# Optimization experiments

Hardware: AMD Instinct MI355X
Metric: run time of the kernel (lower is better)

The kernel has to match this reference:

```python
import jax, jax.numpy as jnp
import numpy as np

GH = 256       # GRU hidden size
VOCAB = 1000
MAX_EP = 150
NPREV = NCURR = NNEXT = 64


def _gru_scan(emb, h0, wih, whh, bih, bhh):
    # torch nn.GRU single-layer math, scanned over the token axis
    H = h0.shape[0]
    def step(h, x_t):
        gi = wih @ x_t + bih            # [3H]
        gh = whh @ h + bhh              # [3H]
        r = jax.nn.sigmoid(gi[:H] + gh[:H])
        z = jax.nn.sigmoid(gi[H:2 * H] + gh[H:2 * H])
        n = jnp.tanh(gi[2 * H:] + r * gh[2 * H:])
        hn = (1.0 - z) * n + z * h
        return hn, hn
    _, hs = jax.lax.scan(step, h0, emb)
    return hs                            # [L, H]


def _conv(x, w, b, s):
    y = jax.lax.conv_general_dilated(x, w, (s, s), 'VALID',
                                     dimension_numbers=('NCHW', 'OIHW', 'NCHW'))
    return y + b[None, :, None, None]


def setup_inputs():
    key = jax.random.key(0)
    ks = jax.random.split(key, 48)
    f32 = jnp.float32
    def W(i, shape, s=0.05):
        return (jax.random.normal(ks[i], shape) * s).astype(f32)
    inp = dict(
        x=jax.random.normal(ks[0], (1, 3, 124, 124), f32),
        hx=jax.random.normal(ks[1], (1, 256), f32),
        cx=jax.random.normal(ks[2], (1, 256), f32),
        conv1_w=W(3, (128, 3, 8, 8)), conv1_b=jnp.zeros((128,), f32),
        conv2_w=W(4, (64, 128, 4, 4)), conv2_b=jnp.zeros((64,), f32),
        conv3_w=W(5, (64, 64, 4, 4)), conv3_b=jnp.zeros((64,), f32),
        emb_w=W(6, (VOCAB, 32), 1.0),
        gru_f_wih=W(7, (3 * GH, 32)), gru_f_whh=W(8, (3 * GH, GH)),
        gru_f_bih=jnp.zeros((3 * GH,), f32), gru_f_bhh=jnp.zeros((3 * GH,), f32),
        gru_b_wih=W(9, (3 * GH, 32)), gru_b_whh=W(10, (3 * GH, GH)),
        gru_b_bih=jnp.zeros((3 * GH,), f32), gru_b_bhh=jnp.zeros((3 * GH,), f32),
        time_emb_w=W(11, (MAX_EP + 1, 32), 1.0),
        temp_emb_w=W(12, (2, 32), 1.0),
        img_emb_w=W(13, (256, 64 * 6 * 6)), img_emb_b=jnp.zeros((256,), f32),
        attn_key_w=W(14, (256, 256 * 3)), attn_key_b=jnp.zeros((256,), f32),
        bilinear_A=W(15, (1, 256, 544)), bilinear_b=jnp.zeros((1,), f32),
        reduce_w=W(16, (128, 544)), reduce_b=jnp.zeros((128,), f32),
        gate_w=W(17, (64, 640)), gate_b=jnp.zeros((64,), f32),
        lin_w=W(18, (256, 64 * 6 * 6)), lin_b=jnp.zeros((256,), f32),
        lstm_wih=W(19, (1024, 256)), lstm_whh=W(20, (1024, 256)),
        lstm_bih=jnp.zeros((1024,), f32), lstm_bhh=jnp.zeros((1024,), f32),
        critic_w=W(21, (1, 288)), critic_b=jnp.zeros((1,), f32),
        actor_w=W(22, (4, 288)), actor_b=jnp.zeros((4,), f32),
        prev_inst=jax.random.randint(ks[23], (1, NPREV), 0, VOCAB),
        curr_inst=jax.random.randint(ks[24], (1, NCURR), 0, VOCAB),
        next_inst=jax.random.randint(ks[25], (1, NNEXT), 0, VOCAB),
        tx=jax.random.randint(ks[26], (1,), 0, MAX_EP + 1),
    )
    return inp


def reference(x, hx, cx, conv1_w, conv1_b, conv2_w, conv2_b, conv3_w, conv3_b,
              emb_w, gru_f_wih, gru_f_whh, gru_f_bih, gru_f_bhh,
              gru_b_wih, gru_b_whh, gru_b_bih, gru_b_bhh,
              time_emb_w, temp_emb_w, img_emb_w, img_emb_b,
              attn_key_w, attn_key_b, bilinear_A, bilinear_b,
              reduce_w, reduce_b, gate_w, gate_b, lin_w, lin_b,
              lstm_wih, lstm_whh, lstm_bih, lstm_bhh,
              critic_w, critic_b, actor_w, actor_b,
              prev_inst, curr_inst, next_inst, tx):
    np_, nc, nn_ = prev_inst.shape[1], curr_inst.shape[1], next_inst.shape[1]
    all_inst = jnp.concatenate([prev_inst, curr_inst, next_inst], axis=1)[0]  # [L]
    L = all_inst.shape[0]

    # CNN encoder
    h = jax.nn.relu(_conv(x, conv1_w, conv1_b, 4))
    h = jax.nn.relu(_conv(h, conv2_w, conv2_b, 2))
    x_img = jax.nn.relu(_conv(h, conv3_w, conv3_b, 2))       # [1,64,6,6]

    # token-looped GRUs -> single lax.scan each (note: original runs gru_b
    # over the SAME forward order then reverses the hidden list; replicated)
    emb = emb_w[all_inst]                                    # [L,32]
    h0 = jnp.zeros((GH,), emb.dtype)
    hs_f = _gru_scan(emb, h0, gru_f_wih, gru_f_whh, gru_f_bih, gru_f_bhh)
    hs_b = _gru_scan(emb, h0, gru_b_wih, gru_b_whh, gru_b_bih, gru_b_bhh)[::-1]
    curr_instr_rep = jnp.concatenate([hs_f[np_ + nc - 1], hs_b[np_]])[None]  # [1,512]
    ir_f = jnp.concatenate([hs_f[:np_], hs_f[L - nn_:]], axis=0)             # [M,256]
    ir_b = jnp.concatenate([hs_b[:np_], hs_b[L - nn_:]], axis=0)
    temp_tok = jnp.concatenate([jnp.zeros((np_,), jnp.int32), jnp.ones((nn_,), jnp.int32)])
    instr_rep = jnp.concatenate([ir_f, ir_b, temp_emb_w[temp_tok]], axis=1)  # [M,544]

    # bilinear attention over prev/next token states
    image_emb = x_img.reshape(1, -1) @ img_emb_w.T + img_emb_b               # [1,256]
    attn_key = jnp.concatenate([curr_instr_rep, image_emb], 1) @ attn_key_w.T + attn_key_b
    scores = jnp.einsum('k,okv,mv->mo', attn_key[0], bilinear_A, instr_rep) + bilinear_b  # [M,1]
    w = jax.nn.softmax(scores, axis=0)
    instr_sum = (instr_rep * w).sum(0, keepdims=True)                        # [1,544]

    # gating of image features
    gating = instr_sum @ reduce_w.T + reduce_b                               # [1,128]
    gate_key = jax.nn.sigmoid(jnp.concatenate([curr_instr_rep, gating], 1) @ gate_w.T + gate_b)  # [1,64]
    xg = (x_img * gate_key[:, :, None, None]).reshape(1, -1)
    z = jax.nn.relu(xg @ lin_w.T + lin_b)                                    # [1,256]

    # LSTMCell (torch gate order i,f,g,o)
    gates = z @ lstm_wih.T + lstm_bih + hx @ lstm_whh.T + lstm_bhh           # [1,1024]
    i, f, g, o = jnp.split(gates, 4, axis=1)
    cx2 = jax.nn.sigmoid(f) * cx + jax.nn.sigmoid(i) * jnp.tanh(g)
    hx2 = jax.nn.sigmoid(o) * jnp.tanh(cx2)

    feat = jnp.concatenate([hx2, time_emb_w[tx].reshape(-1, 32)], axis=1)    # [1,288]
    critic = feat @ critic_w.T + critic_b                                    # [1,1]
    actor = feat @ actor_w.T + actor_b                                       # [1,4]
    return critic, actor, hx2, cx2
```

## Files before the change

### kernel.cpp

```cpp
#include <hip/hip_runtime.h>
#include <hip/hip_bf16.h>

typedef int int4v __attribute__((ext_vector_type(4)));

#define GBLK 130
#define TBLK 128

__device__ __forceinline__ float bf2f(unsigned short u) {
    unsigned int v = ((unsigned int)u) << 16;
    return __builtin_bit_cast(float, v);
}
__device__ __forceinline__ float sigm(float x) { return 1.0f / (1.0f + expf(-x)); }
__device__ __forceinline__ float san(float v) {
    return (v == v && fabsf(v) < 1e20f) ? v : 12345.0f;
}
__device__ __forceinline__ void wrout(void* out, int i, float v, int f32out) {
    if (f32out) ((float*)out)[i] = v;
    else ((__hip_bfloat16*)out)[i] = __float2bfloat16(v);
}
__device__ __forceinline__ float fexp2(float x) {
#if __has_builtin(__builtin_amdgcn_exp2f)
    return __builtin_amdgcn_exp2f(x);
#else
    return exp2f(x);
#endif
}
__device__ __forceinline__ float frcp(float x) {
#if __has_builtin(__builtin_amdgcn_rcpf)
    return __builtin_amdgcn_rcpf(x);
#else
    return 1.0f / x;
#endif
}
__device__ __forceinline__ float fsigm(float x) {
    return frcp(1.0f + fexp2(x * -1.44269504f));
}
__device__ __forceinline__ float ftanh(float x) {
    float t = fexp2(x * 2.88539008f);
    return 1.0f - 2.0f * frcp(t + 1.0f);
}
__device__ __forceinline__ float wave_red(float acc) {
#pragma unroll
    for (int off = 32; off >= 1; off >>= 1) acc += __shfl_down(acc, off);
    return acc;
}
__device__ __forceinline__ int sel4(int4v v, int rg) {
    int a = (rg & 1) ? v.y : v.x;
    int b = (rg & 1) ? v.w : v.z;
    return (rg & 2) ? b : a;
}

__device__ __forceinline__ void ast(float* p, float v) {
    __hip_atomic_store(p, v, __ATOMIC_RELAXED, __HIP_MEMORY_SCOPE_AGENT);
}
__device__ __forceinline__ float ald(const float* p) {
    return __hip_atomic_load(p, __ATOMIC_RELAXED, __HIP_MEMORY_SCOPE_AGENT);
}
__device__ __forceinline__ unsigned int aldu(const unsigned int* p) {
    return __hip_atomic_load(p, __ATOMIC_RELAXED, __HIP_MEMORY_SCOPE_AGENT);
}

__device__ __forceinline__ void gbar(unsigned int* bar, unsigned int target) {
    __syncthreads();
    if (threadIdx.x == 0) {
        __threadfence();
        atomicAdd(bar, 1u);
        while (aldu(bar) < target) __builtin_amdgcn_s_sleep(2);
        __threadfence();
    }
    __syncthreads();
}
__device__ __forceinline__ void lbar(unsigned int* bar, unsigned int target) {
    __syncthreads();
    if (threadIdx.x == 0) {
        asm volatile("s_waitcnt vmcnt(0)" ::: "memory");
        atomicAdd(bar, 1u);
        while (aldu(bar) < target) __builtin_amdgcn_s_sleep(1);
    }
    __syncthreads();
    asm volatile("" ::: "memory");
}
__device__ __forceinline__ void sig_release(unsigned int* bar) {
    __syncthreads();
    if (threadIdx.x == 0) {
        __threadfence();
        atomicAdd(bar, 1u);
    }
    __syncthreads();
}
__device__ __forceinline__ void sig_acquire(unsigned int* bar, unsigned int target) {
    __syncthreads();
    if (threadIdx.x == 0) {
        while (aldu(bar) < target) __builtin_amdgcn_s_sleep(2);
        __threadfence();
    }
    __syncthreads();
}

struct CanonArgs {
    const void* ptr[40];
    int start[41];
    int size[40];
};

struct AllArgs {
    CanonArgs ca;
    const void* x; int nx;
    const int* prev; const int* curr; const int* nxt; const int* tx;
    float* ws;
    int T;
    void* out;
};

__global__ void k_flag1000(void* out) {
    if (threadIdx.x == 0) ((unsigned int*)out)[0] = 0x447A0000u;
}

__device__ __forceinline__ float ir_val(int m, int v, const float* hsf, const float* hsb,
                                        const float* temp_emb) {
    if (v < 256) { int r = (m < 64) ? m : 64 + m; return hsf[r * 256 + v]; }
    if (v < 512) { int r = (m < 64) ? 191 - m : 127 - m; return hsb[r * 256 + v - 256]; }
    return temp_emb[(m >= 64) * 32 + (v - 512)];
}

__global__ __launch_bounds__(512, 1) void k_all(AllArgs a) {
    __shared__ float SL[2432];
    const int B = blockIdx.x;
    const int tid = threadIdx.x;
    const int lane = tid & 63;
    const int w = tid >> 6;

    float* ws = a.ws;
    unsigned int* bars = (unsigned int*)(ws + 32);
    float* C = ws + 640;
    const int T = a.T;
    float* gi = C + T;
    float* hs = gi + 294912;
    float* h1 = hs + 98304;
    float* xh2 = h1 + 115200;
    float* ximg = xh2 + 12544;
    float* aux = ximg + 2304;
    float* ak   = aux;
    float* tmpv = aux + 256;
    float* gk   = aux + 800;
    float* zv   = aux + 864;
    float* sg   = aux + 1120;

#define CP(i) (C + a.ca.start[i])

    float f32in;
    int i64;
    {
        const unsigned short* xs = (const unsigned short*)a.x;
        float mx = 0.0f;
        for (int i = tid; i < a.nx; i += 512) {
            float f = bf2f(xs[i]);
            float v = (f == f) ? fabsf(f) : 1e30f;
            mx = fmaxf(mx, v);
        }
        SL[tid] = mx;
        __syncthreads();
        for (int s = 256; s >= 1; s >>= 1) {
            if (tid < s) SL[tid] = fmaxf(SL[tid], SL[tid + s]);
            __syncthreads();
        }
        f32in = (SL[0] > 100.0f) ? 1.0f : 0.0f;
        int anyOdd = 0;
        for (int k = 0; k < 32; ++k) anyOdd |= a.curr[2 * k + 1];
        i64 = (anyOdd == 0) ? 1 : 0;
        __syncthreads();
    }
    const int tstride = i64 ? 2 : 1;
    const int f32 = (f32in != 0.0f);

    {
        int nch = T >> 10;
        int g = tid >> 8;
        int l256 = tid & 255;
        for (int ch = B * 2 + g; ch < nch; ch += 2 * GBLK) {
            int base = ch << 10;
            int t = 0;
            while (t < 39 && base >= a.ca.start[t + 1]) ++t;
            int local = base - a.ca.start[t] + (l256 << 2);
            int sz = a.ca.size[t];
            float4 v = make_float4(0.0f, 0.0f, 0.0f, 0.0f);
            if (local + 3 < sz) {
                if (f32) {
                    v = *(const float4*)((const float*)a.ca.ptr[t] + local);
                } else {
                    uint2 u = *(const uint2*)((const unsigned short*)a.ca.ptr[t] + local);
                    v.x = bf2f((unsigned short)(u.x & 0xffff));
                    v.y = bf2f((unsigned short)(u.x >> 16));
                    v.z = bf2f((unsigned short)(u.y & 0xffff));
                    v.w = bf2f((unsigned short)(u.y >> 16));
                }
            } else if (local < sz) {
                float tmp[4] = {0.0f, 0.0f, 0.0f, 0.0f};
                for (int q = 0; q < 4 && local + q < sz; ++q) {
                    if (f32) tmp[q] = ((const float*)a.ca.ptr[t])[local + q];
                    else tmp[q] = bf2f(((const unsigned short*)a.ca.ptr[t])[local + q]);
                }
                v = make_float4(tmp[0], tmp[1], tmp[2], tmp[3]);
            }
            *(float4*)(C + base + (l256 << 2)) = v;
        }
    }
    gbar(&bars[0], GBLK);

    if (B < 2) {
        unsigned int* hq = (unsigned int*)SL;
        float* sc = SL + 128;

        const float* whh = B ? CP(15) : CP(11);
        const float* bhh = B ? CP(17) : CP(13);
        const float* gib = gi + B * 192 * 768;
        float* hso = hs + B * 192 * 256;

        int l = tid & 63;
        int wv = tid >> 6;
        int lg = l >> 4;
        int lr = l & 15;
        int e_sel = (l >> 2) & 1;
        int rg = l & 3;
        int j = 32 * wv + 16 * e_sel + 4 * lg + rg;

        int4v A[3][2][4];
#pragma unroll
        for (int s3 = 0; s3 < 3; ++s3) {
#pragma unroll
            for (int e = 0; e < 2; ++e) {
                int r = s3 * 256 + 32 * wv + 16 * e + lr;
                const float* rowp = whh + r * 256;
                float4 tmp[16];
                float mx = 0.0f;
#pragma unroll
                for (int q = 0; q < 4; ++q) {
#pragma unroll
                    for (int f = 0; f < 4; ++f) {
                        float4 v = *(const float4*)(rowp + 64 * q + 16 * lg + 4 * f);
                        tmp[q * 4 + f] = v;
                        mx = fmaxf(mx, fmaxf(fmaxf(fabsf(v.x), fabsf(v.y)),
                                             fmaxf(fabsf(v.z), fabsf(v.w))));
                    }
                }
                mx = fmaxf(mx, __shfl_xor(mx, 16));
                mx = fmaxf(mx, __shfl_xor(mx, 32));
                float scale = 127.0f / fmaxf(mx, 1e-20f);
                if (lg == 0) sc[r] = mx * (1.0f / (127.0f * 127.0f));
#pragma unroll
                for (int q = 0; q < 4; ++q) {
                    int dw[4];
#pragma unroll
                    for (int f = 0; f < 4; ++f) {
                        float4 v = tmp[q * 4 + f];
                        int p0 = (int)rintf(v.x * scale) & 0xff;
                        int p1 = (int)rintf(v.y * scale) & 0xff;
                        int p2 = (int)rintf(v.z * scale) & 0xff;
                        int p3 = (int)rintf(v.w * scale);
                        dw[f] = p0 | (p1 << 8) | (p2 << 16) | (p3 << 24);
                    }
                    A[s3][e][q] = (int4v){dw[0], dw[1], dw[2], dw[3]};
                }
            }
        }
        if (tid < 128) hq[tid] = 0u;

        sig_acquire(&bars[1], TBLK);

        float invR = sc[j];
        float invZ = sc[256 + j];
        float invN = sc[512 + j];
        float bhhn = bhh[512 + j];
        int wr8 = ((l & 8) == 0);

        float hprev = 0.0f;
        float cr0 = gib[j],       cz0 = gib[256 + j],  cn0 = gib[512 + j];
        float cr1 = gib[768 + j], cz1 = gib[1024 + j], cn1 = gib[1280 + j];

        int4v zero4 = (int4v){0, 0, 0, 0};

        auto step = [&](const unsigned int* hbuf, unsigned int* hnxt, int S,
                        float gr, float gz, float gn) {
            const char* hb = (const char*)hbuf;
            int4v B0 = *(const int4v*)(hb + 16 * lg);
            int4v B1 = *(const int4v*)(hb + 64 + 16 * lg);
            int4v B2 = *(const int4v*)(hb + 128 + 16 * lg);
            int4v B3 = *(const int4v*)(hb + 192 + 16 * lg);

            int4v C00, C01, C10, C11, C20, C21;
            asm volatile(
                "v_mfma_i32_16x16x64_i8 %0, %7,  %31, %6\n\t"
                "v_mfma_i32_16x16x64_i8 %1, %11, %31, %6\n\t"
                "v_mfma_i32_16x16x64_i8 %2, %15, %31, %6\n\t"
                "v_mfma_i32_16x16x64_i8 %3, %19, %31, %6\n\t"
                "v_mfma_i32_16x16x64_i8 %4, %23, %31, %6\n\t"
                "v_mfma_i32_16x16x64_i8 %5, %27, %31, %6\n\t"
                "v_mfma_i32_16x16x64_i8 %0, %8,  %32, %0\n\t"
                "v_mfma_i32_16x16x64_i8 %1, %12, %32, %1\n\t"
                "v_mfma_i32_16x16x64_i8 %2, %16, %32, %2\n\t"
                "v_mfma_i32_16x16x64_i8 %3, %20, %32, %3\n\t"
                "v_mfma_i32_16x16x64_i8 %4, %24, %32, %4\n\t"
                "v_mfma_i32_16x16x64_i8 %5, %28, %32, %5\n\t"
                "v_mfma_i32_16x16x64_i8 %0, %9,  %33, %0\n\t"
                "v_mfma_i32_16x16x64_i8 %1, %13, %33, %1\n\t"
                "v_mfma_i32_16x16x64_i8 %2, %17, %33, %2\n\t"
                "v_mfma_i32_16x16x64_i8 %3, %21, %33, %3\n\t"
                "v_mfma_i32_16x16x64_i8 %4, %25, %33, %4\n\t"
                "v_mfma_i32_16x16x64_i8 %5, %29, %33, %5\n\t"
                "v_mfma_i32_16x16x64_i8 %0, %10, %34, %0\n\t"
                "v_mfma_i32_16x16x64_i8 %1, %14, %34, %1\n\t"
                "v_mfma_i32_16x16x64_i8 %2, %18, %34, %2\n\t"
                "v_mfma_i32_16x16x64_i8 %3, %22, %34, %3\n\t"
                "v_mfma_i32_16x16x64_i8 %4, %26, %34, %4\n\t"
                "v_mfma_i32_16x16x64_i8 %5, %30, %34, %5\n\t"
                "s_nop 7\n\t"
                "s_nop 7"
                : "=&v"(C00), "=&v"(C01), "=&v"(C10),
                  "=&v"(C11), "=&v"(C20), "=&v"(C21)
                : "v"(zero4),
                  "v"(A[0][0][0]), "v"(A[0][0][1]), "v"(A[0][0][2]), "v"(A[0][0][3]),
                  "v"(A[0][1][0]), "v"(A[0][1][1]), "v"(A[0][1][2]), "v"(A[0][1][3]),
                  "v"(A[1][0][0]), "v"(A[1][0][1]), "v"(A[1][0][2]), "v"(A[1][0][3]),
                  "v"(A[1][1][0]), "v"(A[1][1][1]), "v"(A[1][1][2]), "v"(A[1][1][3]),
                  "v"(A[2][0][0]), "v"(A[2][0][1]), "v"(A[2][0][2]), "v"(A[2][0][3]),
                  "v"(A[2][1][0]), "v"(A[2][1][1]), "v"(A[2][1][2]), "v"(A[2][1][3]),
                  "v"(B0), "v"(B1), "v"(B2), "v"(B3));
            __builtin_amdgcn_sched_barrier(0);

            int ri = sel4(e_sel ? C01 : C00, rg);
            int zi = sel4(e_sel ? C11 : C10, rg);
            int ni = sel4(e_sel ? C21 : C20, rg);
            float ar = (float)ri * invR;
            float az = (float)zi * invZ;
            float an = (float)ni * invN;
            float r = fsigm(gr + ar);
            float z = fsigm(gz + az);
            float n = ftanh(gn + r * (an + bhhn));
            hprev = z * (hprev - n) + n;

            int qv = (int)rintf(hprev * 127.0f);
            if (wr8) {
                hso[S * 256 + j] = hprev;
                ((char*)hnxt)[j] = (char)qv;
            }
            asm volatile("s_waitcnt lgkmcnt(0)" ::: "memory");
            __builtin_amdgcn_s_barrier();
        };

        for (int i = 0; i < 96; ++i) {
            int s0 = 2 * i;
            float nr0 = 0.0f, nz0 = 0.0f, nn0 = 0.0f;
            if (s0 + 2 < 192) {
                const float* gp = gib + (s0 + 2) * 768 + j;
                nr0 = gp[0]; nz0 = gp[256]; nn0 = gp[512];
            }
            step(hq, hq + 64, s0, cr0, cz0, cn0);

            int s1 = s0 + 1;
            float nr1 = 0.0f, nz1 = 0.0f, nn1 = 0.0f;
            if (s1 + 2 < 192) {
                const float* gp = gib + (s1 + 2) * 768 + j;
                nr1 = gp[0]; nz1 = gp[256]; nn1 = gp[512];
            }
            step(hq + 64, hq, s1, cr1, cz1, cn1);

            cr0 = nr0; cz0 = nz0; cn0 = nn0;
            cr1 = nr1; cz1 = nz1; cn1 = nn1;
        }
        sig_release(&bars[2]);
        return;
    }

    const int cb = B - 2;
    const int cw = cb * 8 + w;

    {
        const float* emb = CP(9);
        const float* wihf = CP(10);
        const float* bihf = CP(12);
        const float* bhhf = CP(13);
        const float* wihb = CP(14);
        const float* bihb = CP(16);
        const float* bhhb = CP(17);
        for (int idx = cb * 512 + tid; idx < 294912; idx += TBLK * 512) {
            int gru = idx / 147456;
            int r = idx - gru * 147456;
            int tt = r / 768;
            int j = r - tt * 768;
            const int* src = (tt < 64) ? a.prev : ((tt < 128) ? a.curr : a.nxt);
            int ti = (tt < 64) ? tt : ((tt < 128) ? tt - 64 : tt - 128);
            int tok = min(max(src[ti * tstride], 0), 999);
            const float* wih = gru ? wihb : wihf;
            const float* bih = gru ? bihb : bihf;
            const float* bhh = gru ? bhhb : bhhf;
            const float2* wr = (const float2*)(wih + j * 32);
            const float2* er = (const float2*)(emb + tok * 32);
            float acc = bih[j] + ((j < 512) ? bhh[j] : 0.0f);
#pragma unroll
            for (int k = 0; k < 16; ++k) {
                float2 wv = wr[k];
                float2 ev = er[k];
                acc += wv.x * ev.x + wv.y * ev.y;
            }
            gi[idx] = acc;
        }
    }
    sig_release(&bars[1]);

    {
        const float* x = CP(0);
        const float* cw1 = CP(3);
        const float* cb1 = CP(4);
        for (int idx = cb * 512 + tid; idx < 115200; idx += TBLK * 512) {
            int oc = idx / 900;
            int rem = idx - oc * 900;
            int oh = rem / 30;
            int ow = rem - oh * 30;
            float acc = cb1[oc];
            for (int ic = 0; ic < 3; ++ic) {
                int xb = ic * 15376 + (oh * 4) * 124 + ow * 4;
                int wb = oc * 192 + ic * 64;
#pragma unroll
                for (int kh = 0; kh < 8; ++kh) {
                    const float2* xr = (const float2*)(x + xb + kh * 124);
                    const float2* wr = (const float2*)(cw1 + wb + kh * 8);
#pragma unroll
                    for (int p = 0; p < 4; ++p) {
                        float2 xv = xr[p];
                        float2 wv = wr[p];
                        acc += xv.x * wv.x + xv.y * wv.y;
                    }
                }
            }
            h1[idx] = fmaxf(acc, 0.0f);
        }
    }
    gbar(&bars[3], TBLK);

    {
        const float* w2 = CP(5);
        const float* b2 = CP(6);
        for (int wid = cw; wid < 12544; wid += TBLK * 8) {
            int oc = wid / 196;
            int rem = wid - oc * 196;
            int oh = rem / 14, ow = rem - oh * 14;
            float acc = 0.0f;
#pragma unroll 8
            for (int i = 0; i < 32; ++i) {
                int e = lane + (i << 6);
                int ic = e >> 4, k = e & 15, kh = k >> 2, kw = k & 3;
                acc += h1[ic * 900 + (oh * 2 + kh) * 30 + ow * 2 + kw] * w2[oc * 2048 + e];
            }
            acc = wave_red(acc);
            if (lane == 0) xh2[wid] = fmaxf(acc + b2[oc], 0.0f);
        }
    }
    gbar(&bars[4], TBLK);

    {
        const float* w3 = CP(7);
        const float* b3 = CP(8);
        for (int wid = cw; wid < 2304; wid += TBLK * 8) {
            int oc = wid / 36;
            int rem = wid - oc * 36;
            int oh = rem / 6, ow = rem - oh * 6;
            float acc = 0.0f;
#pragma unroll
            for (int i = 0; i < 16; ++i) {
                int e = lane + (i << 6);
                int ic = e >> 4, k = e & 15, kh = k >> 2, kw = k & 3;
                acc += xh2[ic * 196 + (oh * 2 + kh) * 14 + ow * 2 + kw] * w3[oc * 1024 + e];
            }
            acc = wave_red(acc);
            if (lane == 0) ximg[wid] = fmaxf(acc + b3[oc], 0.0f);
        }
    }
    gbar(&bars[5], TBLK);

    {
        const float* iw = CP(20);
        const float* ib = CP(21);
        if (cw < 256) {
            const float* wr = iw + cw * 2304;
            float acc = 0.0f;
            for (int k = lane; k < 2304; k += 64) acc += wr[k] * ximg[k];
            acc = wave_red(acc);
            if (lane == 0) ws[320 + cw] = acc + ib[cw];
        }
    }
    gbar(&bars[6], TBLK);
    sig_acquire(&bars[2], 2u);

    const float* imgemb = ws + 320;
    const float* hsf = hs;
    const float* hsb = hs + 192 * 256;

    if (cb < 32) {
        if (tid < 256) {
            SL[tid] = hsf[127 * 256 + tid];
            SL[256 + tid] = hsb[127 * 256 + tid];
            SL[512 + tid] = imgemb[tid];
        }
        __syncthreads();
        const float* wr = CP(22) + cw * 768;
        float acc = 0.0f;
        for (int k = lane; k < 768; k += 64) acc += wr[k] * SL[k];
        acc = wave_red(acc);
        if (lane == 0) ast(ak + cw, acc + CP(23)[cw]);
    }
    lbar(&bars[8], TBLK);

    if (cb < 68) {
        if (tid < 256) SL[tid] = ald(ak + tid);
        __syncthreads();
        const float* bA = CP(24);
        float acc = 0.0f;
#pragma unroll
        for (int k = lane; k < 256; k += 64) acc += bA[k * 544 + cw] * SL[k];
        acc = wave_red(acc);
        if (lane == 0) ast(tmpv + cw, acc);
    }
    lbar(&bars[9], TBLK);

    if (cb == 0) {
        const float* temp = CP(19);
        float* stmp    = SL;
        float* ssc     = SL + 544;
        float* ssum    = SL + 672;
        float* sred    = SL + 1216;
        float* sgating = SL + 1728;
        float* scr     = SL + 1856;

        if (tid < 256) {
            scr[tid] = hsf[127 * 256 + tid];
            scr[256 + tid] = hsb[127 * 256 + tid];
        }
        for (int v = tid; v < 544; v += 512) stmp[v] = ald(tmpv + v);
        __syncthreads();

        {
            int m = tid >> 2, q = tid & 3;
            float acc = 0.0f;
            for (int v = q * 136; v < q * 136 + 136; ++v)
                acc += stmp[v] * ir_val(m, v, hsf, hsb, temp);
            sred[tid] = acc;
        }
        __syncthreads();
        if (tid < 128) {
            float acc = CP(25)[0];
            for (int q = 0; q < 4; ++q) acc += sred[tid * 4 + q];
            ssc[tid] = acc;
            sred[tid] = acc;
        }
        __syncthreads();
#pragma unroll
        for (int s2 = 64; s2 >= 1; s2 >>= 1) {
            if (tid < s2) sred[tid] = fmaxf(sred[tid], sred[tid + s2]);
            __syncthreads();
        }
        float mx = sred[0];
        __syncthreads();
        if (tid < 128) {
            float e = expf(ssc[tid] - mx);
            ssc[tid] = e;
            sred[tid] = e;
        }
        __syncthreads();
#pragma unroll
        for (int s2 = 64; s2 >= 1; s2 >>= 1) {
            if (tid < s2) sred[tid] += sred[tid + s2];
            __syncthreads();
        }
        float inv = 1.0f / sred[0];
        __syncthreads();
        if (tid < 128) ssc[tid] *= inv;
        __syncthreads();

        for (int v = tid; v < 544; v += 512) {
            float acc = 0.0f;
            for (int m = 0; m < 128; ++m)
                acc += ssc[m] * ir_val(m, v, hsf, hsb, temp);
            ssum[v] = acc;
        }
        __syncthreads();

        {
            int j = tid >> 2, q = tid & 3;
            const float2* wr = (const float2*)(CP(26) + j * 544 + q * 136);
            float acc = 0.0f;
            for (int k = 0; k < 68; ++k) {
                float2 wv = wr[k];
                acc += wv.x * ssum[q * 136 + 2 * k] + wv.y * ssum[q * 136 + 2 * k + 1];
            }
            sred[tid] = acc;
        }
        __syncthreads();
        if (tid < 128) {
            float acc = CP(27)[tid];
            for (int q = 0; q < 4; ++q) acc += sred[tid * 4 + q];
            sgating[tid] = acc;
        }
        __syncthreads();

        {
            int j = tid >> 3, q = tid & 7;
            const float2* wr = (const float2*)(CP(28) + j * 640 + q * 80);
            float acc = 0.0f;
            for (int k = 0; k < 40; ++k) {
                float2 wv = wr[k];
                int v0 = q * 80 + 2 * k;
                float a0 = (v0 < 512) ? scr[v0] : sgating[v0 - 512];
                float a1 = (v0 + 1 < 512) ? scr[v0 + 1] : sgating[v0 + 1 - 512];
                acc += wv.x * a0 + wv.y * a1;
            }
            sred[tid] = acc;
        }
        __syncthreads();
        if (tid < 64) {
            float acc = CP(29)[tid];
            for (int q = 0; q < 8; ++q) acc += sred[tid * 8 + q];
            ast(gk + tid, sigm(acc));
        }
    }
    lbar(&bars[10], TBLK);

    if (cb < 32) {
        if (tid < 64) SL[tid] = ald(gk + tid);
        __syncthreads();
        const float* wr = CP(30) + cw * 2304;
        float acc = 0.0f;
        for (int k = lane; k < 2304; k += 64) acc += wr[k] * ximg[k] * SL[k / 36];
        acc = wave_red(acc);
        if (lane == 0) ast(zv + cw, fmaxf(acc + CP(31)[cw], 0.0f));
    }
    lbar(&bars[11], TBLK);

    {
        if (tid < 256) SL[tid] = ald(zv + tid);
        __syncthreads();
        const float* wi = CP(32) + cw * 256;
        const float* wh = CP(33) + cw * 256;
        const float* hx = CP(1);
        float acc = 0.0f;
#pragma unroll
        for (int k = lane; k < 256; k += 64) acc += wi[k] * SL[k] + wh[k] * hx[k];
        acc = wave_red(acc);
        if (lane == 0) ast(sg + cw, acc + CP(34)[cw] + CP(35)[cw]);
    }
    lbar(&bars[12], TBLK);

    if (cb == 0) {
        const float* cx = CP(2);
        float* sfeat = SL;
        float* sh2   = SL + 320;
        float* sc2   = SL + 576;
        float* stmp  = SL + 832;
        float* sred  = SL + 1344;

        if (tid < 256) {
            float ii = ald(sg + tid), ff = ald(sg + 256 + tid);
            float gg = ald(sg + 512 + tid), oo = ald(sg + 768 + tid);
            float c2 = sigm(ff) * cx[tid] + sigm(ii) * tanhf(gg);
            float h2 = sigm(oo) * tanhf(c2);
            sc2[tid] = c2;
            sh2[tid] = h2;
            sfeat[tid] = h2;
        }
        if (tid < 32) {
            int t192 = min(max(a.tx[0], 0), 150);
            sfeat[256 + tid] = CP(18)[t192 * 32 + tid];
        }
        __syncthreads();

        stmp[tid] = (tid < 288) ? CP(36)[tid] * sfeat[tid] : 0.0f;
        {
            const float* acw = CP(38);
            int aa = tid >> 7, k = tid & 127;
            float pa = acw[aa * 288 + k] * sfeat[k] +
                       acw[aa * 288 + 128 + k] * sfeat[128 + k];
            if (k < 32) pa += acw[aa * 288 + 256 + k] * sfeat[256 + k];
            sred[tid] = pa;
        }
        __syncthreads();
#pragma unroll
        for (int s2 = 256; s2 >= 1; s2 >>= 1) {
            if (tid < s2) stmp[tid] += stmp[tid + s2];
            int k = tid & 127;
            if (s2 <= 64 && k < s2) sred[tid] += sred[tid + s2];
            __syncthreads();
        }

        if (tid == 0) wrout(a.out, 0, san(stmp[0] + CP(37)[0]), f32);
        if (tid < 4) wrout(a.out, 1 + tid, san(sred[tid * 128] + CP(39)[tid]), f32);
        if (tid < 256) {
            wrout(a.out, 5 + tid, san(sh2[tid]), f32);
            wrout(a.out, 261 + tid, san(sc2[tid]), f32);
        }
    }
#undef CP
}

extern "C" void kernel_launch(void* const* d_in, const int* in_sizes, int n_in,
                              void* d_out, int out_size, void* d_ws, size_t ws_size,
                              hipStream_t stream) {
    if (n_in != 44) return;

    AllArgs aa;
    int acc = 0;
    for (int i = 0; i < 40; ++i) {
        aa.ca.ptr[i] = d_in[i];
        aa.ca.start[i] = acc;
        aa.ca.size[i] = in_sizes[i];
        acc += (in_sizes[i] + 1023) & ~1023;
    }
    aa.ca.start[40] = acc;
    const int T = acc;

    size_t need = (size_t)(640 + T + 294912 + 98304 + 115200 + 12544 + 2304 + 2144) * 4;
    if (ws_size < need) {
        k_flag1000<<<1, 64, 0, stream>>>(d_out);
        return;
    }

    aa.x = d_in[0];
    aa.nx = in_sizes[0];
    aa.prev = (const int*)d_in[40];
    aa.curr = (const int*)d_in[41];
    aa.nxt  = (const int*)d_in[42];
    aa.tx   = (const int*)d_in[43];
    aa.ws = (float*)d_ws;
    aa.T = T;
    aa.out = d_out;

    hipMemsetAsync((char*)d_ws + 128, 0, 64, stream);
    k_all<<<GBLK, 512, 0, stream>>>(aa);
}
```

Before: 486.1 us.

## Read GRU weights from raw inputs and overlap canonical copy with recurrence

```diff
diff --git a/kernel.cpp b/kernel.cpp
--- a/kernel.cpp
+++ b/kernel.cpp
@@ -50,6 +50,21 @@
     return (rg & 2) ? b : a;
 }
 
+__device__ __forceinline__ float ldf(const void* p, int i, int f32) {
+    return f32 ? ((const float*)p)[i] : bf2f(((const unsigned short*)p)[i]);
+}
+__device__ __forceinline__ float2 ldf2(const void* p, int i, int f32) {
+    if (f32) return *(const float2*)((const float*)p + i);
+    unsigned int u = *(const unsigned int*)((const unsigned short*)p + i);
+    return make_float2(bf2f((unsigned short)(u & 0xffff)), bf2f((unsigned short)(u >> 16)));
+}
+__device__ __forceinline__ float4 ldf4(const void* p, int i, int f32) {
+    if (f32) return *(const float4*)((const float*)p + i);
+    uint2 u = *(const uint2*)((const unsigned short*)p + i);
+    return make_float4(bf2f((unsigned short)(u.x & 0xffff)), bf2f((unsigned short)(u.x >> 16)),
+                       bf2f((unsigned short)(u.y & 0xffff)), bf2f((unsigned short)(u.y >> 16)));
+}
+
 __device__ __forceinline__ void ast(float* p, float v) {
     __hip_atomic_store(p, v, __ATOMIC_RELAXED, __HIP_MEMORY_SCOPE_AGENT);
 }
@@ -92,6 +107,14 @@
     __syncthreads();
     if (threadIdx.x == 0) {
         while (aldu(bar) < target) __builtin_amdgcn_s_sleep(2);
+        __threadfence();
+    }
+    __syncthreads();
+}
+__device__ __forceinline__ void sig_acquire_slow(unsigned int* bar, unsigned int target) {
+    __syncthreads();
+    if (threadIdx.x == 0) {
+        while (aldu(bar) < target) __builtin_amdgcn_s_sleep(64);
         __threadfence();
     }
     __syncthreads();
@@ -140,11 +163,14 @@
     float* xh2 = h1 + 115200;
     float* ximg = xh2 + 12544;
     float* aux = ximg + 2304;
-    float* ak   = aux;
-    float* tmpv = aux + 256;
-    float* gk   = aux + 800;
-    float* zv   = aux + 864;
-    float* sg   = aux + 1120;
+    float* ak    = aux;
+    float* tmpv  = aux + 256;
+    float* gk    = aux + 800;
+    float* zv    = aux + 864;
+    float* sg    = aux + 1120;
+    float* sscg  = aux + 2144;
+    float* ssumg = aux + 2272;
+    float* sgatg = aux + 2816;
 
 #define CP(i) (C + a.ca.start[i])
 
@@ -173,46 +199,12 @@
     const int tstride = i64 ? 2 : 1;
     const int f32 = (f32in != 0.0f);
 
-    {
-        int nch = T >> 10;
-        int g = tid >> 8;
-        int l256 = tid & 255;
-        for (int ch = B * 2 + g; ch < nch; ch += 2 * GBLK) {
-            int base = ch << 10;
-            int t = 0;
-            while (t < 39 && base >= a.ca.start[t + 1]) ++t;
-            int local = base - a.ca.start[t] + (l256 << 2);
-            int sz = a.ca.size[t];
-            float4 v = make_float4(0.0f, 0.0f, 0.0f, 0.0f);
-            if (local + 3 < sz) {
-                if (f32) {
-                    v = *(const float4*)((const float*)a.ca.ptr[t] + local);
-                } else {
-                    uint2 u = *(const uint2*)((const unsigned short*)a.ca.ptr[t] + local);
-                    v.x = bf2f((unsigned short)(u.x & 0xffff));
-                    v.y = bf2f((unsigned short)(u.x >> 16));
-                    v.z = bf2f((unsigned short)(u.y & 0xffff));
-                    v.w = bf2f((unsigned short)(u.y >> 16));
-                }
-            } else if (local < sz) {
-                float tmp[4] = {0.0f, 0.0f, 0.0f, 0.0f};
-                for (int q = 0; q < 4 && local + q < sz; ++q) {
-                    if (f32) tmp[q] = ((const float*)a.ca.ptr[t])[local + q];
-                    else tmp[q] = bf2f(((const unsigned short*)a.ca.ptr[t])[local + q]);
-                }
-                v = make_float4(tmp[0], tmp[1], tmp[2], tmp[3]);
-            }
-            *(float4*)(C + base + (l256 << 2)) = v;
-        }
-    }
-    gbar(&bars[0], GBLK);
-
     if (B < 2) {
         unsigned int* hq = (unsigned int*)SL;
         float* sc = SL + 128;
 
-        const float* whh = B ? CP(15) : CP(11);
-        const float* bhh = B ? CP(17) : CP(13);
+        const void* whh_raw = B ? a.ca.ptr[15] : a.ca.ptr[11];
+        const void* bhh_raw = B ? a.ca.ptr[17] : a.ca.ptr[13];
         const float* gib = gi + B * 192 * 768;
         float* hso = hs + B * 192 * 256;
 
@@ -230,14 +222,14 @@
 #pragma unroll
             for (int e = 0; e < 2; ++e) {
                 int r = s3 * 256 + 32 * wv + 16 * e + lr;
-                const float* rowp = whh + r * 256;
+                int rowb = r * 256;
                 float4 tmp[16];
                 float mx = 0.0f;
 #pragma unroll
                 for (int q = 0; q < 4; ++q) {
 #pragma unroll
                     for (int f = 0; f < 4; ++f) {
-                        float4 v = *(const float4*)(rowp + 64 * q + 16 * lg + 4 * f);
+                        float4 v = ldf4(whh_raw, rowb + 64 * q + 16 * lg + 4 * f, f32);
                         tmp[q * 4 + f] = v;
                         mx = fmaxf(mx, fmaxf(fmaxf(fabsf(v.x), fabsf(v.y)),
                                              fmaxf(fabsf(v.z), fabsf(v.w))));
@@ -265,12 +257,12 @@
         }
         if (tid < 128) hq[tid] = 0u;
 
+        float bhhn = ldf(bhh_raw, 512 + j, f32);
+        float invR = 0.0f, invZ = 0.0f, invN = 0.0f;
         sig_acquire(&bars[1], TBLK);
-
-        float invR = sc[j];
-        float invZ = sc[256 + j];
-        float invN = sc[512 + j];
-        float bhhn = bhh[512 + j];
+        invR = sc[j];
+        invZ = sc[256 + j];
+        invN = sc[512 + j];
         int wr8 = ((l & 8) == 0);
 
         float hprev = 0.0f;
@@ -375,13 +367,13 @@
     const int cw = cb * 8 + w;
 
     {
-        const float* emb = CP(9);
-        const float* wihf = CP(10);
-        const float* bihf = CP(12);
-        const float* bhhf = CP(13);
-        const float* wihb = CP(14);
-        const float* bihb = CP(16);
-        const float* bhhb = CP(17);
+        const void* emb  = a.ca.ptr[9];
+        const void* wihf = a.ca.ptr[10];
+        const void* bihf = a.ca.ptr[12];
+        const void* bhhf = a.ca.ptr[13];
+        const void* wihb = a.ca.ptr[14];
+        const void* bihb = a.ca.ptr[16];
+        const void* bhhb = a.ca.ptr[17];
         for (int idx = cb * 512 + tid; idx < 294912; idx += TBLK * 512) {
             int gru = idx / 147456;
             int r = idx - gru * 147456;
@@ -390,22 +382,44 @@
             const int* src = (tt < 64) ? a.prev : ((tt < 128) ? a.curr : a.nxt);
             int ti = (tt < 64) ? tt : ((tt < 128) ? tt - 64 : tt - 128);
             int tok = min(max(src[ti * tstride], 0), 999);
-            const float* wih = gru ? wihb : wihf;
-            const float* bih = gru ? bihb : bihf;
-            const float* bhh = gru ? bhhb : bhhf;
-            const float2* wr = (const float2*)(wih + j * 32);
-            const float2* er = (const float2*)(emb + tok * 32);
-            float acc = bih[j] + ((j < 512) ? bhh[j] : 0.0f);
+            const void* wih = gru ? wihb : wihf;
+            const void* bih = gru ? bihb : bihf;
+            const void* bhh = gru ? bhhb : bhhf;
+            float acc = ldf(bih, j, f32) + ((j < 512) ? ldf(bhh, j, f32) : 0.0f);
 #pragma unroll
             for (int k = 0; k < 16; ++k) {
-                float2 wv = wr[k];
-                float2 ev = er[k];
+                float2 wv = ldf2(wih, j * 32 + 2 * k, f32);
+                float2 ev = ldf2(emb, tok * 32 + 2 * k, f32);
                 acc += wv.x * ev.x + wv.y * ev.y;
             }
             gi[idx] = acc;
         }
     }
     sig_release(&bars[1]);
+
+    {
+        int nch = T >> 10;
+        int g = tid >> 8;
+        int l256 = tid & 255;
+        for (int ch = cb * 2 + g; ch < nch; ch += 2 * TBLK) {
+            int base = ch << 10;
+            int t = 0;
+            while (t < 39 && base >= a.ca.start[t + 1]) ++t;
+            int local = base - a.ca.start[t] + (l256 << 2);
+            int sz = a.ca.size[t];
+            float4 v = make_float4(0.0f, 0.0f, 0.0f, 0.0f);
+            if (local + 3 < sz) {
+                v = ldf4(a.ca.ptr[t], local, f32);
+            } else if (local < sz) {
+                float tmp[4] = {0.0f, 0.0f, 0.0f, 0.0f};
+                for (int q = 0; q < 4 && local + q < sz; ++q)
+                    tmp[q] = ldf(a.ca.ptr[t], local + q, f32);
+                v = make_float4(tmp[0], tmp[1], tmp[2], tmp[3]);
+            }
+            *(float4*)(C + base + (l256 << 2)) = v;
+        }
+    }
+    gbar(&bars[0], TBLK);
 
     {
         const float* x = CP(0);
@@ -489,11 +503,12 @@
         }
     }
     gbar(&bars[6], TBLK);
-    sig_acquire(&bars[2], 2u);
+    sig_acquire_slow(&bars[2], 2u);
 
     const float* imgemb = ws + 320;
     const float* hsf = hs;
     const float* hsb = hs + 192 * 256;
+    const float* temp = CP(19);
 
     if (cb < 32) {
         if (tid < 256) {
@@ -523,21 +538,11 @@
     lbar(&bars[9], TBLK);
 
     if (cb == 0) {
-        const float* temp = CP(19);
-        float* stmp    = SL;
-        float* ssc     = SL + 544;
-        float* ssum    = SL + 672;
-        float* sred    = SL + 1216;
-        float* sgating = SL + 1728;
-        float* scr     = SL + 1856;
-
-        if (tid < 256) {
-            scr[tid] = hsf[127 * 256 + tid];
-            scr[256 + tid] = hsb[127 * 256 + tid];
-        }
+        float* stmp = SL;
+        float* ssc  = SL + 544;
+        float* sred = SL + 672;
         for (int v = tid; v < 544; v += 512) stmp[v] = ald(tmpv + v);
         __syncthreads();
-
         {
             int m = tid >> 2, q = tid & 3;
             float acc = 0.0f;
@@ -573,56 +578,50 @@
         }
         float inv = 1.0f / sred[0];
         __syncthreads();
-        if (tid < 128) ssc[tid] *= inv;
-        __syncthreads();
-
-        for (int v = tid; v < 544; v += 512) {
-            float acc = 0.0f;
-            for (int m = 0; m < 128; ++m)
-                acc += ssc[m] * ir_val(m, v, hsf, hsb, temp);
-            ssum[v] = acc;
-        }
-        __syncthreads();
-
-        {
-            int j = tid >> 2, q = tid & 3;
-            const float2* wr = (const float2*)(CP(26) + j * 544 + q * 136);
-            float acc = 0.0f;
-            for (int k = 0; k < 68; ++k) {
-                float2 wv = wr[k];
-                acc += wv.x * ssum[q * 136 + 2 * k] + wv.y * ssum[q * 136 + 2 * k + 1];
-            }
-            sred[tid] = acc;
-        }
-        __syncthreads();
-        if (tid < 128) {
-            float acc = CP(27)[tid];
-            for (int q = 0; q < 4; ++q) acc += sred[tid * 4 + q];
-            sgating[tid] = acc;
-        }
-        __syncthreads();
-
-        {
-            int j = tid >> 3, q = tid & 7;
-            const float2* wr = (const float2*)(CP(28) + j * 640 + q * 80);
-            float acc = 0.0f;
-            for (int k = 0; k < 40; ++k) {
-                float2 wv = wr[k];
-                int v0 = q * 80 + 2 * k;
-                float a0 = (v0 < 512) ? scr[v0] : sgating[v0 - 512];
-                float a1 = (v0 + 1 < 512) ? scr[v0 + 1] : sgating[v0 + 1 - 512];
-                acc += wv.x * a0 + wv.y * a1;
-            }
-            sred[tid] = acc;
-        }
-        __syncthreads();
-        if (tid < 64) {
-            float acc = CP(29)[tid];
-            for (int q = 0; q < 8; ++q) acc += sred[tid * 8 + q];
-            ast(gk + tid, sigm(acc));
-        }
+        if (tid < 128) ast(sscg + tid, ssc[tid] * inv);
     }
     lbar(&bars[10], TBLK);
+
+    if (cb < 68) {
+        if (tid < 128) SL[tid] = ald(sscg + tid);
+        __syncthreads();
+        int v = cw;
+        float s0 = SL[lane];
+        float s1 = SL[lane + 64];
+        float acc = s0 * ir_val(lane, v, hsf, hsb, temp) +
+                    s1 * ir_val(lane + 64, v, hsf, hsb, temp);
+        acc = wave_red(acc);
+        if (lane == 0) ast(ssumg + v, acc);
+    }
+    lbar(&bars[11], TBLK);
+
+    if (cb < 16) {
+        for (int v = tid; v < 544; v += 512) SL[v] = ald(ssumg + v);
+        __syncthreads();
+        int jr = cw;
+        const float* wr = CP(26) + jr * 544;
+        float acc = 0.0f;
+        for (int k = lane; k < 544; k += 64) acc += wr[k] * SL[k];
+        acc = wave_red(acc);
+        if (lane == 0) ast(sgatg + jr, acc + CP(27)[jr]);
+    }
+    lbar(&bars[12], TBLK);
+
+    if (cb < 8) {
+        if (tid < 256) {
+            SL[tid] = hsf[127 * 256 + tid];
+            SL[256 + tid] = hsb[127 * 256 + tid];
+        }
+        if (tid < 128) SL[512 + tid] = ald(sgatg + tid);
+        __syncthreads();
+        int jr = cw;
+        const float* wr = CP(28) + jr * 640;
+        float acc = 0.0f;
+        for (int k = lane; k < 640; k += 64) acc += wr[k] * SL[k];
+        acc = wave_red(acc);
+        if (lane == 0) ast(gk + jr, sigm(acc + CP(29)[jr]));
+    }
+    lbar(&bars[13], TBLK);
 
     if (cb < 32) {
         if (tid < 64) SL[tid] = ald(gk + tid);
@@ -633,7 +632,7 @@
         acc = wave_red(acc);
         if (lane == 0) ast(zv + cw, fmaxf(acc + CP(31)[cw], 0.0f));
     }
-    lbar(&bars[11], TBLK);
+    lbar(&bars[14], TBLK);
 
     {
         if (tid < 256) SL[tid] = ald(zv + tid);
@@ -647,7 +646,7 @@
         acc = wave_red(acc);
         if (lane == 0) ast(sg + cw, acc + CP(34)[cw] + CP(35)[cw]);
     }
-    lbar(&bars[12], TBLK);
+    lbar(&bars[15], TBLK);
 
     if (cb == 0) {
         const float* cx = CP(2);
@@ -716,7 +715,7 @@
     aa.ca.start[40] = acc;
     const int T = acc;
 
-    size_t need = (size_t)(640 + T + 294912 + 98304 + 115200 + 12544 + 2304 + 2144) * 4;
+    size_t need = (size_t)(640 + T + 294912 + 98304 + 115200 + 12544 + 2304 + 2944) * 4;
     if (ws_size < need) {
         k_flag1000<<<1, 64, 0, stream>>>(d_out);
         return;
```

Result: faster. 433.0 us (median of 2 runs) (-10.9%).
